# Kernel optimization log

Hardware: AMD Instinct MI355X
Metric: run time of the kernel (lower is better)

Reference implementation:

```python
import jax, jax.numpy as jnp
import numpy as np

N = 50000   # nodes
E = 400000  # edges
H = 128     # num_hidden


def _glorot(key, shape):
    fan_in, fan_out = shape
    lim = float(np.sqrt(6.0 / (fan_in + fan_out)))
    return jax.random.uniform(key, shape, jnp.float32, -lim, lim)


def setup_inputs() -> dict:
    key = jax.random.key(0)
    ks = jax.random.split(key, 16)
    x = jax.random.normal(ks[0], (N, H), jnp.float32)
    pos = jax.random.normal(ks[1], (N, 3), jnp.float32)
    pe = jax.random.normal(ks[2], (N, H), jnp.float32)
    send = jax.random.randint(ks[3], (E,), 0, N)
    # avoid self-loops so dist > 0 (torch.norm grad at 0 is NaN; same hazard in jax)
    off = jax.random.randint(ks[4], (E,), 1, N)
    rec = (send + off) % N
    edge_index = jnp.stack([send, rec]).astype(jnp.int64)
    # message_mlp: Linear(4H+1, H) -> SiLU -> Linear(H, H) -> SiLU
    W1 = _glorot(ks[5], (4 * H + 1, H)); b1 = jnp.zeros((H,), jnp.float32)
    W2 = _glorot(ks[6], (H, H));          b2 = jnp.zeros((H,), jnp.float32)
    # message_mlp_pos: Linear(2H+1, H) -> Tanh -> Linear(H, H) -> Tanh
    Wp1 = _glorot(ks[7], (2 * H + 1, H)); bp1 = jnp.zeros((H,), jnp.float32)
    Wp2 = _glorot(ks[8], (H, H));          bp2 = jnp.zeros((H,), jnp.float32)
    return {"x": x, "pos": pos, "pe": pe, "edge_index": edge_index,
            "W1": W1, "b1": b1, "W2": W2, "b2": b2,
            "Wp1": Wp1, "bp1": bp1, "Wp2": Wp2, "bp2": bp2}


def reference(x, pos, pe, edge_index, W1, b1, W2, b2, Wp1, bp1, Wp2, bp2):
    send, rec = edge_index[0], edge_index[1]
    # gather node + pe features along edges
    dist = jnp.linalg.norm(pos[send] - pos[rec], axis=1, keepdims=True)  # [E,1]
    state = jnp.concatenate([x[send], pe[send], x[rec], pe[rec], dist], axis=1)  # [E,4H+1]
    state_pe = jnp.concatenate([pe[send], pe[rec], dist], axis=1)                 # [E,2H+1]
    # edge MLPs
    msg = jax.nn.silu(jax.nn.silu(state @ W1 + b1) @ W2 + b2)      # [E,H]
    msg_pe = jnp.tanh(jnp.tanh(state_pe @ Wp1 + bp1) @ Wp2 + bp2)  # [E,H]
    # scatter_add aggregate to receiving nodes
    aggr = jax.ops.segment_sum(msg, rec, num_segments=x.shape[0])
    aggr_pe = jax.ops.segment_sum(msg_pe, rec, num_segments=x.shape[0])
    # residual updates
    return x + aggr, pe + aggr_pe
```

## Files before the change

kernel.cpp:

```cpp
#include <hip/hip_runtime.h>
#include <stdint.h>

#define N_NODES 50000
#define NE      400000
#define HDIM    128
#define MPAD    50048
#define TE      128
#define NTILE   (NE / TE)
#define SCAN_BS 512
#define SCAN_NB 98

typedef __attribute__((ext_vector_type(8))) short bf16x8;
typedef __attribute__((ext_vector_type(4))) float f32x4;

__device__ __forceinline__ ushort f2b(float f) {
    uint32_t u = __float_as_uint(f);
    uint32_t r = (u + 0x7fffu + ((u >> 16) & 1u)) >> 16;
    return (ushort)r;
}
__device__ __forceinline__ float b2f(ushort s) {
    return __uint_as_float(((uint32_t)s) << 16);
}
__device__ __forceinline__ uint32_t cvtpk(float lo, float hi) {
    uint32_t r;
    asm("v_cvt_pk_bf16_f32 %0, %1, %2" : "=v"(r) : "v"(lo), "v"(hi));
    return r;
}

__device__ __forceinline__ float silu_f(float x) {
    return x * __builtin_amdgcn_rcpf(1.f + __expf(-x));
}
__device__ __forceinline__ float tanh_f(float x) {
    return fmaf(-2.f, __builtin_amdgcn_rcpf(1.f + __expf(2.f * x)), 1.f);
}

__global__ void k_prep_nodes(const float4* __restrict__ x, const float4* __restrict__ pe,
                             const int* __restrict__ cov,
                             ushort* __restrict__ Xc, float4* __restrict__ out) {
    int idx = blockIdx.x * 256 + threadIdx.x;
    int row = idx >> 6;
    int cq  = idx & 63;
    float4 v = make_float4(0.f, 0.f, 0.f, 0.f);
    if (row < N_NODES) {
        bool wr = (cov[row] == 0);
        if (cq < 32) { v = x[row * 32 + cq];          if (wr) out[row * 32 + cq] = v; }
        else         { v = pe[row * 32 + (cq - 32)];  if (wr) out[N_NODES * 32 + row * 32 + (cq - 32)] = v; }
    }
    ushort r[4] = { f2b(v.x), f2b(v.y), f2b(v.z), f2b(v.w) };
    *(uint2*)(Xc + (size_t)row * 256 + cq * 4) = *(const uint2*)r;
}

__global__ void k_prep_w(const float* __restrict__ W1, const float* __restrict__ Wp1,
                         const float* __restrict__ W2, const float* __restrict__ Wp2,
                         ushort* __restrict__ WcT, ushort* __restrict__ W2t,
                         ushort* __restrict__ Wp2t, float* __restrict__ w1d,
                         float* __restrict__ wp1d) {
    int b = blockIdx.x, t = threadIdx.x;
    if (b < 512) {
        int n = b, k = t;
        float v;
        if (n < 128)       v = W1[k * HDIM + n];
        else if (n < 256)  v = W1[(256 + k) * HDIM + (n - 128)];
        else if (n < 384)  v = (k < 128) ? 0.f : Wp1[(k - 128) * HDIM + (n - 256)];
        else               v = (k < 128) ? 0.f : Wp1[k * HDIM + (n - 384)];
        WcT[n * 256 + k] = f2b(v);
    } else if (b < 640) {
        if (t < 128) { int n = b - 512; W2t[n * HDIM + t] = f2b(W2[t * HDIM + n]); }
    } else if (b < 768) {
        if (t < 128) { int n = b - 640; Wp2t[n * HDIM + t] = f2b(Wp2[t * HDIM + n]); }
    } else {
        if (t < 128) w1d[t] = W1[512 * HDIM + t];
        else if (t < 256) wp1d[t - 128] = Wp1[256 * HDIM + (t - 128)];
    }
}

__global__ void k_hist(const int* __restrict__ eidx, int* __restrict__ cnt) {
    int e = blockIdx.x * 256 + threadIdx.x;
    if (e < NE) atomicAdd(&cnt[eidx[NE + e]], 1);
}

__global__ __launch_bounds__(SCAN_BS) void k_scan1(const int* __restrict__ cnt,
                                                   int* __restrict__ locs,
                                                   int* __restrict__ sums) {
    __shared__ int sh[SCAN_BS];
    int tid = threadIdx.x;
    int i = blockIdx.x * SCAN_BS + tid;
    int v = (i < N_NODES) ? cnt[i] : 0;
    sh[tid] = v;
    __syncthreads();
    for (int off = 1; off < SCAN_BS; off <<= 1) {
        int t = (tid >= off) ? sh[tid - off] : 0;
        __syncthreads();
        sh[tid] += t;
        __syncthreads();
    }
    locs[i] = sh[tid];
    if (tid == SCAN_BS - 1) sums[blockIdx.x] = sh[tid];
}

__global__ void k_scan2(int* __restrict__ sums) {
    __shared__ int sh[128];
    int tid = threadIdx.x;
    sh[tid] = (tid < SCAN_NB) ? sums[tid] : 0;
    __syncthreads();
    for (int off = 1; off < 128; off <<= 1) {
        int t = (tid >= off) ? sh[tid - off] : 0;
        __syncthreads();
        sh[tid] += t;
        __syncthreads();
    }
    if (tid < SCAN_NB) sums[tid] = sh[tid];
}

__global__ __launch_bounds__(SCAN_BS) void k_scan3(const int* __restrict__ cnt,
                                                   const int* __restrict__ locs,
                                                   const int* __restrict__ sums,
                                                   int* __restrict__ start,
                                                   int* __restrict__ cursor,
                                                   int* __restrict__ nodeCov) {
    int tid = threadIdx.x, b = blockIdx.x;
    int i = b * SCAN_BS + tid;
    if (i > N_NODES) return;
    int base = b ? sums[b - 1] : 0;
    int v = (i < N_NODES) ? cnt[i] : 0;
    int ex = base + locs[i] - v;
    start[i] = ex;
    if (i < N_NODES) {
        cursor[i] = ex;
        int covered = (v > 0) && ((ex >> 7) == ((ex + v - 1) >> 7));
        nodeCov[i] = covered;
    }
}

__global__ void k_place(const int* __restrict__ eidx, const float* __restrict__ pos,
                        int* __restrict__ cursor, int* __restrict__ sendS,
                        int* __restrict__ recS, float* __restrict__ distS) {
    int e = blockIdx.x * 256 + threadIdx.x;
    if (e >= NE) return;
    int s = eidx[e], r = eidx[NE + e];
    int p = atomicAdd(&cursor[r], 1);
    sendS[p] = s; recS[p] = r;
    float dx = pos[s * 3 + 0] - pos[r * 3 + 0];
    float dy = pos[s * 3 + 1] - pos[r * 3 + 1];
    float dz = pos[s * 3 + 2] - pos[r * 3 + 2];
    distS[p] = sqrtf(dx * dx + dy * dy + dz * dz);
}

__global__ __launch_bounds__(128) void k_segmeta(const int* __restrict__ recS,
                                                 const int* __restrict__ startA,
                                                 const int* __restrict__ cntA,
                                                 uint32_t* __restrict__ tileSegs,
                                                 int* __restrict__ segCnt) {
    __shared__ int sR[128];
    __shared__ int sFlag[128];
    __shared__ int sStart[129];
    int tid = threadIdx.x;
    int t0 = blockIdx.x * 128;
    sR[tid] = recS[t0 + tid];
    __syncthreads();
    int f = (tid == 0) || (sR[tid] != sR[tid - 1]);
    sFlag[tid] = f;
    __syncthreads();
    for (int off = 1; off < 128; off <<= 1) {
        int v = (tid >= off) ? sFlag[tid - off] : 0;
        __syncthreads();
        sFlag[tid] += v;
        __syncthreads();
    }
    int nSeg = sFlag[127];
    if (f) sStart[sFlag[tid] - 1] = tid;
    if (tid == 0) { sStart[nSeg] = 128; segCnt[blockIdx.x] = nSeg; }
    __syncthreads();
    if (f) {
        int seg = sFlag[tid] - 1;
        int r0 = tid;
        int len = sStart[seg + 1] - r0;
        int n = sR[r0];
        int g0 = t0 + r0;
        int st = startA[n];
        uint32_t interior = (g0 == st) && (g0 + len == st + cntA[n]);
        tileSegs[(size_t)blockIdx.x * 128 + seg] =
            (uint32_t)r0 | ((uint32_t)(len - 1) << 7) | (interior << 14) | ((uint32_t)n << 16);
    }
}

__global__ __launch_bounds__(256) void k_node_gemm(const ushort* __restrict__ Xc,
                                                   const ushort* __restrict__ WcT,
                                                   ushort* __restrict__ Pn) {
    const int m0 = blockIdx.y * 128;
    const int n0 = blockIdx.x * 128;
    const int wave = threadIdx.x >> 6;
    const int lane = threadIdx.x & 63;
    const int l15 = lane & 15, quad = lane >> 4;
    const int qr = (wave >> 1) * 64, qc = (wave & 1) * 64;

    f32x4 acc[4][4];
#pragma unroll
    for (int i = 0; i < 4; i++)
#pragma unroll
        for (int j = 0; j < 4; j++) acc[i][j] = (f32x4){0.f, 0.f, 0.f, 0.f};

#pragma unroll
    for (int s = 0; s < 8; s++) {
        const int k0 = s * 32 + quad * 8;
        bf16x8 a[4], b[4];
#pragma unroll
        for (int rg = 0; rg < 4; rg++) {
            int row = m0 + qr + rg * 16 + l15;
            a[rg] = *(const bf16x8*)(Xc + row * 256 + k0);
        }
#pragma unroll
        for (int cg = 0; cg < 4; cg++) {
            int nn = n0 + qc + cg * 16 + l15;
            b[cg] = *(const bf16x8*)(WcT + nn * 256 + k0);
        }
#pragma unroll
        for (int rg = 0; rg < 4; rg++)
#pragma unroll
            for (int cg = 0; cg < 4; cg++)
                acc[rg][cg] = __builtin_amdgcn_mfma_f32_16x16x32_bf16(a[rg], b[cg], acc[rg][cg], 0, 0, 0);
    }

#pragma unroll
    for (int rg = 0; rg < 4; rg++)
#pragma unroll
        for (int cg = 0; cg < 4; cg++) {
            int col = n0 + qc + cg * 16 + l15;
            int rowb = m0 + qr + rg * 16 + quad * 4;
            uint32_t p01 = cvtpk(acc[rg][cg][0], acc[rg][cg][1]);
            uint32_t p23 = cvtpk(acc[rg][cg][2], acc[rg][cg][3]);
            Pn[(size_t)(rowb + 0) * 512 + col] = (ushort)p01;
            Pn[(size_t)(rowb + 1) * 512 + col] = (ushort)(p01 >> 16);
            Pn[(size_t)(rowb + 2) * 512 + col] = (ushort)p23;
            Pn[(size_t)(rowb + 3) * 512 + col] = (ushort)(p23 >> 16);
        }
}

__global__ __launch_bounds__(256, 4) void k_fused(
    const ushort* __restrict__ Pn,
    const int* __restrict__ sendS, const int* __restrict__ recS,
    const float* __restrict__ distS,
    const uint32_t* __restrict__ tileSegs, const int* __restrict__ segCntA,
    const float* __restrict__ w1d, const float* __restrict__ wp1d,
    const float* __restrict__ b1, const float* __restrict__ bp1,
    const ushort* __restrict__ W2t, const ushort* __restrict__ Wp2t,
    const float* __restrict__ b2, const float* __restrict__ bp2,
    const float* __restrict__ x, const float* __restrict__ pe,
    float* __restrict__ out)
{
    __shared__ __align__(16) ushort sA[TE * 128];
    __shared__ int sS[TE];
    __shared__ int sR[TE];
    __shared__ float sD[TE];
    __shared__ uint32_t sSeg[TE];

    const int tid = threadIdx.x;
    const int tile = blockIdx.x;
    const int p = blockIdx.y;
    const int t0 = tile * TE;

    if (tid < TE) {
        sS[tid] = sendS[t0 + tid];
        sR[tid] = recS[t0 + tid];
        sD[tid] = distS[t0 + tid];
    } else {
        sSeg[tid - TE] = tileSegs[(size_t)tile * TE + (tid - TE)];
    }
    const int nSeg = segCntA[tile];

    const int g = tid >> 4, c = tid & 15;
    const float* wd = p ? wp1d : w1d;
    const float* bb = p ? bp1 : b1;
    float4 wv0 = *(const float4*)(wd + c * 8);
    float4 wv1 = *(const float4*)(wd + c * 8 + 4);
    float4 bv0 = *(const float4*)(bb + c * 8);
    float4 bv1 = *(const float4*)(bb + c * 8 + 4);
    float wva[8] = { wv0.x, wv0.y, wv0.z, wv0.w, wv1.x, wv1.y, wv1.z, wv1.w };
    float bva[8] = { bv0.x, bv0.y, bv0.z, bv0.w, bv1.x, bv1.y, bv1.z, bv1.w };
    __syncthreads();

    {
        const ushort* PnS = Pn + p * 256 + c * 8;
        const ushort* PnR = Pn + p * 256 + 128 + c * 8;
        uint4 us[8], ur[8];
#pragma unroll
        for (int e = 0; e < 8; e++) {
            int el = g * 8 + e;
            us[e] = *(const uint4*)(PnS + (size_t)sS[el] * 512);
            ur[e] = *(const uint4*)(PnR + (size_t)sR[el] * 512);
        }
#define L1_BODY(ACT)                                                        \
        for (int e = 0; e < 8; e++) {                                       \
            int el = g * 8 + e;                                             \
            float d = sD[el];                                               \
            const ushort* pus = (const ushort*)&us[e];                      \
            const ushort* pur = (const ushort*)&ur[e];                      \
            float vv[8];                                                    \
            _Pragma("unroll")                                               \
            for (int j = 0; j < 8; j++) {                                   \
                float v = b2f(pus[j]) + b2f(pur[j]) + d * wva[j] + bva[j];  \
                vv[j] = ACT(v);                                             \
            }                                                               \
            uint4 res;                                                      \
            res.x = cvtpk(vv[0], vv[1]);                                    \
            res.y = cvtpk(vv[2], vv[3]);                                    \
            res.z = cvtpk(vv[4], vv[5]);                                    \
            res.w = cvtpk(vv[6], vv[7]);                                    \
            *(uint4*)(sA + el * 128 + ((c ^ (el & 15)) * 8)) = res;         \
        }
        if (p) {
#pragma unroll
            L1_BODY(tanh_f)
        } else {
#pragma unroll
            L1_BODY(silu_f)
        }
#undef L1_BODY
    }
    __syncthreads();

    const int wave = tid >> 6, lane = tid & 63;
    const int l15 = lane & 15, quad = lane >> 4;
    const ushort* Wt = p ? Wp2t : W2t;

    f32x4 acc[2][8];
#pragma unroll
    for (int rg = 0; rg < 2; rg++)
#pragma unroll
        for (int cg = 0; cg < 8; cg++) acc[rg][cg] = (f32x4){0.f, 0.f, 0.f, 0.f};

#pragma unroll
    for (int s4 = 0; s4 < 4; s4++) {
        int cidx = s4 * 4 + quad;
        int row0 = wave * 32 + l15;
        bf16x8 a0 = *(const bf16x8*)(sA + row0 * 128 + ((cidx ^ l15) * 8));
        bf16x8 a1 = *(const bf16x8*)(sA + (row0 + 16) * 128 + ((cidx ^ l15) * 8));
        int k0 = cidx * 8;
#pragma unroll
        for (int cg = 0; cg < 8; cg++) {
            bf16x8 b = *(const bf16x8*)(Wt + (cg * 16 + l15) * HDIM + k0);
            acc[0][cg] = __builtin_amdgcn_mfma_f32_16x16x32_bf16(a0, b, acc[0][cg], 0, 0, 0);
            acc[1][cg] = __builtin_amdgcn_mfma_f32_16x16x32_bf16(a1, b, acc[1][cg], 0, 0, 0);
        }
    }
    __syncthreads();

    const float* bb2 = p ? bp2 : b2;
#define EPI_BODY(ACT)                                                       \
    for (int rg = 0; rg < 2; rg++) {                                        \
        int rowb = wave * 32 + rg * 16 + quad * 4;                          \
        _Pragma("unroll")                                                   \
        for (int cg = 0; cg < 8; cg++) {                                    \
            int col = cg * 16 + l15;                                        \
            float bias = bb2[col];                                          \
            float e0 = ACT(acc[rg][cg][0] + bias);                          \
            float e1 = ACT(acc[rg][cg][1] + bias);                          \
            float e2 = ACT(acc[rg][cg][2] + bias);                          \
            float e3 = ACT(acc[rg][cg][3] + bias);                          \
            uint32_t p01 = cvtpk(e0, e1);                                   \
            uint32_t p23 = cvtpk(e2, e3);                                   \
            sA[(rowb + 0) * 128 + col] = (ushort)p01;                       \
            sA[(rowb + 1) * 128 + col] = (ushort)(p01 >> 16);               \
            sA[(rowb + 2) * 128 + col] = (ushort)p23;                       \
            sA[(rowb + 3) * 128 + col] = (ushort)(p23 >> 16);               \
        }                                                                   \
    }
    if (p) {
#pragma unroll
        EPI_BODY(tanh_f)
    } else {
#pragma unroll
        EPI_BODY(silu_f)
    }
#undef EPI_BODY
    __syncthreads();

    const float* basep = p ? pe : x;
    float* outb = out + (size_t)p * N_NODES * HDIM;
    for (int task = tid; task < nSeg * 64; task += 256) {
        int seg = task >> 6, cp = task & 63;
        uint32_t wseg = sSeg[seg];
        int r0  = wseg & 127;
        int len = ((wseg >> 7) & 127) + 1;
        int n   = wseg >> 16;
        float a0 = 0.f, a1 = 0.f;
        for (int rr = r0; rr < r0 + len; rr++) {
            unsigned int u = *(const unsigned int*)&sA[rr * 128 + cp * 2];
            a0 += b2f((ushort)(u & 0xffffu));
            a1 += b2f((ushort)(u >> 16));
        }
        float* op = outb + (size_t)n * HDIM + cp * 2;
        if ((wseg >> 14) & 1) {
            float2 bv = *(const float2*)(basep + (size_t)n * HDIM + cp * 2);
            *(float2*)op = make_float2(bv.x + a0, bv.y + a1);
        } else {
            atomicAdd(op, a0);
            atomicAdd(op + 1, a1);
        }
    }
}

extern "C" void kernel_launch(void* const* d_in, const int* in_sizes, int n_in,
                              void* d_out, int out_size, void* d_ws, size_t ws_size,
                              hipStream_t stream) {
    const float* x   = (const float*)d_in[0];
    const float* pos = (const float*)d_in[1];
    const float* pe  = (const float*)d_in[2];
    const int* eidx  = (const int*)d_in[3];
    const float* W1  = (const float*)d_in[4];
    const float* b1  = (const float*)d_in[5];
    const float* W2  = (const float*)d_in[6];
    const float* b2  = (const float*)d_in[7];
    const float* Wp1 = (const float*)d_in[8];
    const float* bp1 = (const float*)d_in[9];
    const float* Wp2 = (const float*)d_in[10];
    const float* bp2 = (const float*)d_in[11];
    float* out = (float*)d_out;

    char* w = (char*)d_ws;
    size_t off = 0;
    ushort* Xc   = (ushort*)(w + off); off += (size_t)MPAD * 256 * 2;
    ushort* Pn   = (ushort*)(w + off); off += (size_t)MPAD * 512 * 2;
    ushort* WcT  = (ushort*)(w + off); off += 512 * 256 * 2;
    ushort* W2t  = (ushort*)(w + off); off += 32768;
    ushort* Wp2t = (ushort*)(w + off); off += 32768;
    float*  w1d  = (float*)(w + off);  off += 2048;
    float*  wp1d = (float*)(w + off);  off += 2048;
    int* cnt     = (int*)(w + off);    off += 200704;
    int* startA  = (int*)(w + off);    off += 200704;
    int* cursor  = (int*)(w + off);    off += 200704;
    int* locs    = (int*)(w + off);    off += 200704;
    int* sums    = (int*)(w + off);    off += 512;
    int* sendS   = (int*)(w + off);    off += (size_t)NE * 4;
    int* recS    = (int*)(w + off);    off += (size_t)NE * 4;
    float* distS = (float*)(w + off);  off += (size_t)NE * 4;
    uint32_t* tileSegs = (uint32_t*)(w + off); off += (size_t)NTILE * 128 * 4;
    int* segCntA = (int*)(w + off);    off += (size_t)NTILE * 4;
    int* nodeCov = (int*)(w + off);    off += 200704;

    hipMemsetAsync(cnt, 0, (N_NODES + 1) * sizeof(int), stream);
    k_hist<<<(NE + 255) / 256, 256, 0, stream>>>(eidx, cnt);
    k_scan1<<<SCAN_NB, SCAN_BS, 0, stream>>>(cnt, locs, sums);
    k_scan2<<<1, 128, 0, stream>>>(sums);
    k_scan3<<<SCAN_NB, SCAN_BS, 0, stream>>>(cnt, locs, sums, startA, cursor, nodeCov);
    k_place<<<(NE + 255) / 256, 256, 0, stream>>>(eidx, pos, cursor, sendS, recS, distS);
    k_segmeta<<<NTILE, 128, 0, stream>>>(recS, startA, cnt, tileSegs, segCntA);

    k_prep_w<<<769, 256, 0, stream>>>(W1, Wp1, W2, Wp2, WcT, W2t, Wp2t, w1d, wp1d);
    k_prep_nodes<<<MPAD / 4, 256, 0, stream>>>((const float4*)x, (const float4*)pe,
                                               nodeCov, Xc, (float4*)out);

    dim3 ggrid(4, MPAD / 128);
    k_node_gemm<<<ggrid, 256, 0, stream>>>(Xc, WcT, Pn);

    dim3 fgrid(NTILE, 2);
    k_fused<<<fgrid, 256, 0, stream>>>(Pn, sendS, recS, distS, tileSegs, segCntA,
                                       w1d, wp1d, b1, bp1, W2t, Wp2t, b2, bp2,
                                       x, pe, out);
}
```

Baseline: 383.3 us.

## Merge prep kernels, use ballot-based segment metadata, XCD-remap node GEMM blocks

Merges the weight-prep and node-prep kernels into one launch by dispatching on block index, which removes one kernel launch. Rewrites the segment-metadata kernel to use wavefront ballots and popcount instead of a shared-memory prefix scan with many barriers. Flattens the node GEMM grid to one dimension and remaps block IDs so that consecutive tiles land on the same XCD, aiming for better L2 reuse of shared input rows. The three pieces are independent small tweaks to auxiliary kernels.

```diff
diff --git a/kernel.cpp b/kernel.cpp
--- a/kernel.cpp
+++ b/kernel.cpp
@@ -34,10 +34,35 @@
     return fmaf(-2.f, __builtin_amdgcn_rcpf(1.f + __expf(2.f * x)), 1.f);
 }
 
-__global__ void k_prep_nodes(const float4* __restrict__ x, const float4* __restrict__ pe,
-                             const int* __restrict__ cov,
-                             ushort* __restrict__ Xc, float4* __restrict__ out) {
-    int idx = blockIdx.x * 256 + threadIdx.x;
+__global__ void k_prep(const float* __restrict__ W1, const float* __restrict__ Wp1,
+                       const float* __restrict__ W2, const float* __restrict__ Wp2,
+                       ushort* __restrict__ WcT, ushort* __restrict__ W2t,
+                       ushort* __restrict__ Wp2t, float* __restrict__ w1d,
+                       float* __restrict__ wp1d,
+                       const float4* __restrict__ x, const float4* __restrict__ pe,
+                       const int* __restrict__ cov,
+                       ushort* __restrict__ Xc, float4* __restrict__ out) {
+    int b = blockIdx.x, t = threadIdx.x;
+    if (b < 769) {
+        if (b < 512) {
+            int n = b, k = t;
+            float v;
+            if (n < 128)       v = W1[k * HDIM + n];
+            else if (n < 256)  v = W1[(256 + k) * HDIM + (n - 128)];
+            else if (n < 384)  v = (k < 128) ? 0.f : Wp1[(k - 128) * HDIM + (n - 256)];
+            else               v = (k < 128) ? 0.f : Wp1[k * HDIM + (n - 384)];
+            WcT[n * 256 + k] = f2b(v);
+        } else if (b < 640) {
+            if (t < 128) { int n = b - 512; W2t[n * HDIM + t] = f2b(W2[t * HDIM + n]); }
+        } else if (b < 768) {
+            if (t < 128) { int n = b - 640; Wp2t[n * HDIM + t] = f2b(Wp2[t * HDIM + n]); }
+        } else {
+            if (t < 128) w1d[t] = W1[512 * HDIM + t];
+            else if (t < 256) wp1d[t - 128] = Wp1[256 * HDIM + (t - 128)];
+        }
+        return;
+    }
+    int idx = (b - 769) * 256 + t;
     int row = idx >> 6;
     int cq  = idx & 63;
     float4 v = make_float4(0.f, 0.f, 0.f, 0.f);
@@ -48,30 +73,6 @@
     }
     ushort r[4] = { f2b(v.x), f2b(v.y), f2b(v.z), f2b(v.w) };
     *(uint2*)(Xc + (size_t)row * 256 + cq * 4) = *(const uint2*)r;
-}
-
-__global__ void k_prep_w(const float* __restrict__ W1, const float* __restrict__ Wp1,
-                         const float* __restrict__ W2, const float* __restrict__ Wp2,
-                         ushort* __restrict__ WcT, ushort* __restrict__ W2t,
-                         ushort* __restrict__ Wp2t, float* __restrict__ w1d,
-                         float* __restrict__ wp1d) {
-    int b = blockIdx.x, t = threadIdx.x;
-    if (b < 512) {
-        int n = b, k = t;
-        float v;
-        if (n < 128)       v = W1[k * HDIM + n];
-        else if (n < 256)  v = W1[(256 + k) * HDIM + (n - 128)];
-        else if (n < 384)  v = (k < 128) ? 0.f : Wp1[(k - 128) * HDIM + (n - 256)];
-        else               v = (k < 128) ? 0.f : Wp1[k * HDIM + (n - 384)];
-        WcT[n * 256 + k] = f2b(v);
-    } else if (b < 640) {
-        if (t < 128) { int n = b - 512; W2t[n * HDIM + t] = f2b(W2[t * HDIM + n]); }
-    } else if (b < 768) {
-        if (t < 128) { int n = b - 640; Wp2t[n * HDIM + t] = f2b(Wp2[t * HDIM + n]); }
-    } else {
-        if (t < 128) w1d[t] = W1[512 * HDIM + t];
-        else if (t < 256) wp1d[t - 128] = Wp1[256 * HDIM + (t - 128)];
-    }
 }
 
 __global__ void k_hist(const int* __restrict__ eidx, int* __restrict__ cnt) {
@@ -151,44 +152,44 @@
                                                  const int* __restrict__ cntA,
                                                  uint32_t* __restrict__ tileSegs,
                                                  int* __restrict__ segCnt) {
-    __shared__ int sR[128];
-    __shared__ int sFlag[128];
-    __shared__ int sStart[129];
+    __shared__ unsigned long long sMask[2];
     int tid = threadIdx.x;
     int t0 = blockIdx.x * 128;
-    sR[tid] = recS[t0 + tid];
-    __syncthreads();
-    int f = (tid == 0) || (sR[tid] != sR[tid - 1]);
-    sFlag[tid] = f;
-    __syncthreads();
-    for (int off = 1; off < 128; off <<= 1) {
-        int v = (tid >= off) ? sFlag[tid - off] : 0;
-        __syncthreads();
-        sFlag[tid] += v;
-        __syncthreads();
-    }
-    int nSeg = sFlag[127];
-    if (f) sStart[sFlag[tid] - 1] = tid;
-    if (tid == 0) { sStart[nSeg] = 128; segCnt[blockIdx.x] = nSeg; }
-    __syncthreads();
+    int r = recS[t0 + tid];
+    int f = (tid == 0) ? 1 : (r != recS[t0 + tid - 1]);
+    int wv = tid >> 6, lane = tid & 63;
+    unsigned long long m = __ballot(f);
+    if (lane == 0) sMask[wv] = m;
+    __syncthreads();
+    unsigned long long m0 = sMask[0], m1 = sMask[1];
+    int total0 = __popcll(m0);
+    if (tid == 0) segCnt[blockIdx.x] = total0 + __popcll(m1);
     if (f) {
-        int seg = sFlag[tid] - 1;
-        int r0 = tid;
-        int len = sStart[seg + 1] - r0;
-        int n = sR[r0];
-        int g0 = t0 + r0;
-        int st = startA[n];
-        uint32_t interior = (g0 == st) && (g0 + len == st + cntA[n]);
+        unsigned long long below = m & ((1ull << lane) - 1ull);
+        int seg = __popcll(below) + (wv ? total0 : 0);
+        unsigned long long higher = (lane == 63) ? 0ull : (m >> (lane + 1));
+        int next;
+        if (higher)       next = tid + 1 + __builtin_ctzll(higher);
+        else if (wv == 0) next = m1 ? 64 + __builtin_ctzll(m1) : 128;
+        else              next = 128;
+        int len = next - tid;
+        int g0 = t0 + tid;
+        int st = startA[r];
+        uint32_t interior = (g0 == st) && (g0 + len == st + cntA[r]);
         tileSegs[(size_t)blockIdx.x * 128 + seg] =
-            (uint32_t)r0 | ((uint32_t)(len - 1) << 7) | (interior << 14) | ((uint32_t)n << 16);
+            (uint32_t)tid | ((uint32_t)(len - 1) << 7) | (interior << 14) | ((uint32_t)r << 16);
     }
 }
 
 __global__ __launch_bounds__(256) void k_node_gemm(const ushort* __restrict__ Xc,
                                                    const ushort* __restrict__ WcT,
                                                    ushort* __restrict__ Pn) {
-    const int m0 = blockIdx.y * 128;
-    const int n0 = blockIdx.x * 128;
+    const int bid = blockIdx.x;
+    const int q = 195, r4 = 4;
+    const int xcd = bid & 7, j = bid >> 3;
+    const int orig = (xcd < r4 ? xcd * (q + 1) : r4 * (q + 1) + (xcd - r4) * q) + j;
+    const int m0 = (orig >> 2) * 128;
+    const int n0 = (orig & 3) * 128;
     const int wave = threadIdx.x >> 6;
     const int lane = threadIdx.x & 63;
     const int l15 = lane & 15, quad = lane >> 4;
@@ -198,7 +199,7 @@
 #pragma unroll
     for (int i = 0; i < 4; i++)
 #pragma unroll
-        for (int j = 0; j < 4; j++) acc[i][j] = (f32x4){0.f, 0.f, 0.f, 0.f};
+        for (int jj = 0; jj < 4; jj++) acc[i][jj] = (f32x4){0.f, 0.f, 0.f, 0.f};
 
 #pragma unroll
     for (int s = 0; s < 8; s++) {
@@ -446,12 +447,12 @@
     k_place<<<(NE + 255) / 256, 256, 0, stream>>>(eidx, pos, cursor, sendS, recS, distS);
     k_segmeta<<<NTILE, 128, 0, stream>>>(recS, startA, cnt, tileSegs, segCntA);
 
-    k_prep_w<<<769, 256, 0, stream>>>(W1, Wp1, W2, Wp2, WcT, W2t, Wp2t, w1d, wp1d);
-    k_prep_nodes<<<MPAD / 4, 256, 0, stream>>>((const float4*)x, (const float4*)pe,
-                                               nodeCov, Xc, (float4*)out);
-
-    dim3 ggrid(4, MPAD / 128);
-    k_node_gemm<<<ggrid, 256, 0, stream>>>(Xc, WcT, Pn);
+    k_prep<<<769 + MPAD / 4, 256, 0, stream>>>(W1, Wp1, W2, Wp2, WcT, W2t, Wp2t,
+                                               w1d, wp1d, (const float4*)x,
+                                               (const float4*)pe, nodeCov, Xc,
+                                               (float4*)out);
+
+    k_node_gemm<<<1564, 256, 0, stream>>>(Xc, WcT, Pn);
 
     dim3 fgrid(NTILE, 2);
     k_fused<<<fgrid, 256, 0, stream>>>(Pn, sendS, recS, distS, tileSegs, segCntA,
```

Measured after the change: 378.3 us. Within noise of the previous version (-1.3%).
